# Kernel tuning notes

Measured on AMD Instinct MI355X. Metric: run time of the kernel, lower is better.

## Reference

```python
import jax, jax.numpy as jnp
import numpy as np

N_VERTS = 200000
NNZ = 1600000
C_IN = 128
C_OUT = 128


def setup_inputs() -> dict:
    key = jax.random.key(0)
    k1, k2, k3, k4, k5, k6 = jax.random.split(key, 6)
    x = jax.random.normal(k1, (N_VERTS, C_IN), dtype=jnp.float32)
    rows = jax.random.randint(k2, (NNZ,), 0, N_VERTS, dtype=jnp.int64)
    cols = jax.random.randint(k3, (NNZ,), 0, N_VERTS, dtype=jnp.int64)
    vals = jax.random.normal(k4, (NNZ,), dtype=jnp.float32)
    W = jax.random.normal(k5, (C_OUT, C_IN), dtype=jnp.float32) * (1.0 / np.sqrt(C_IN))
    b = jax.random.normal(k6, (C_OUT,), dtype=jnp.float32) * 0.01
    return {"x": x, "rows": rows, "cols": cols, "vals": vals, "W": W, "b": b}


def reference(x, rows, cols, vals, W, b):
    # SpMM: out[r] += vals[e] * x[cols[e]]  (F = 2I - L in COO form)
    n = x.shape[0]
    agg = jax.ops.segment_sum(vals[:, None] * x[cols], rows, num_segments=n)  # [N, C_in]
    # Dense Linear projection: agg @ W^T + b
    return agg @ W.T + b  # [N, C_out]
```

## Files before the change

### kernel.cpp

```cpp
#include <hip/hip_runtime.h>

#define NV 200000
#define NE 1600000
#define CD 128
#define NBUCK 3125
#define NBLK 64
#define CHUNK 25600

#define Y_OFF      0UL
#define CNT_OFF    51232768UL
#define TOT_OFF    52032768UL
#define START_OFF  52045312UL
#define SCAT_OFF   52058112UL
#define ROWOFF_OFF 64858112UL
#define SCAT2_OFF  65658368UL

typedef short  short8 __attribute__((ext_vector_type(8)));
typedef float  f32x4  __attribute__((ext_vector_type(4)));

__device__ __forceinline__ unsigned bf16pair(float a, float b) {
    unsigned ua = __float_as_uint(a);
    unsigned ub = __float_as_uint(b);
    ua += 0x7fffu + ((ua >> 16) & 1u);
    ub += 0x7fffu + ((ub >> 16) & 1u);
    return (ua >> 16) | (ub & 0xffff0000u);
}

__device__ __forceinline__ short bf16of(float f) {
    __bf16 h = (__bf16)f;
    return __builtin_bit_cast(short, h);
}

#define PC_BLOCKS 64
#define GEMM_BLOCKS 512
#define GEMM_WAVES (GEMM_BLOCKS * 4)
#define NTILES (NV / 16)

__global__ __launch_bounds__(256, 2) void gemm_pc(const float* __restrict__ x,
                                                  const float* __restrict__ Wm,
                                                  unsigned short* __restrict__ y,
                                                  const int* __restrict__ rows,
                                                  int* __restrict__ cnt) {
    __shared__ __align__(16) char smem[32768];
    const int t = threadIdx.x;

    if (blockIdx.x < PC_BLOCKS) {
        int* hist = reinterpret_cast<int*>(smem);
        const int blk = blockIdx.x;
        for (int i = t; i < NBUCK; i += 256) hist[i] = 0;
        __syncthreads();
        const int e0 = blk * CHUNK;
        const int e1 = min(NE, e0 + CHUNK);
        for (int e = e0 + t; e < e1; e += 256)
            atomicAdd(&hist[rows[e] >> 6], 1);
        __syncthreads();
        for (int i = t; i < NBUCK; i += 256)
            cnt[(size_t)blk * NBUCK + i] = hist[i];
        return;
    }

    short* Wlds = reinterpret_cast<short*>(smem);
    const int lane = t & 63;
    const int w = t >> 6;
    const int g = lane >> 4;

    {
        const float4* Wf4 = reinterpret_cast<const float4*>(Wm);
        uint4* L = reinterpret_cast<uint4*>(Wlds);
#pragma unroll
        for (int i = 0; i < 8; ++i) {
            int c = t + i * 256;
            int l = c & 63;
            int ks = (c >> 6) & 3;
            int tl = c >> 8;
            int row = 16 * tl + (l & 15);
            int j = ks * 4 + (l >> 4);
            float4 wa = Wf4[row * 32 + j * 2];
            float4 wb = Wf4[row * 32 + j * 2 + 1];
            uint4 u;
            u.x = bf16pair(wa.x, wa.y);
            u.y = bf16pair(wa.z, wa.w);
            u.z = bf16pair(wb.x, wb.y);
            u.w = bf16pair(wb.z, wb.w);
            L[c] = u;
        }
    }
    __syncthreads();

    short8 A[8][4];
    {
        const short8* L8 = reinterpret_cast<const short8*>(Wlds);
#pragma unroll
        for (int t8 = 0; t8 < 8; ++t8)
#pragma unroll
            for (int ks = 0; ks < 4; ++ks)
                A[t8][ks] = L8[(t8 * 4 + ks) * 64 + lane];
    }

    const int wgid = (blockIdx.x - PC_BLOCKS) * 4 + w;
    char* yb = reinterpret_cast<char*>(y);

    for (int tile = wgid; tile < NTILES; tile += GEMM_WAVES) {
        const int v0 = tile * 16;
        const int row = v0 + (lane & 15);
        const float4* xr = reinterpret_cast<const float4*>(x + (size_t)row * CD);

        float4 xf[8];
#pragma unroll
        for (int ks = 0; ks < 4; ++ks) {
            xf[2 * ks]     = xr[8 * ks + 2 * g];
            xf[2 * ks + 1] = xr[8 * ks + 2 * g + 1];
        }

        f32x4 acc[8];
#pragma unroll
        for (int t8 = 0; t8 < 8; ++t8) acc[t8] = (f32x4){0.f, 0.f, 0.f, 0.f};

#pragma unroll
        for (int ks = 0; ks < 4; ++ks) {
            short8 B;
            const float* f = reinterpret_cast<const float*>(&xf[2 * ks]);
#pragma unroll
            for (int j = 0; j < 8; ++j) B[j] = bf16of(f[j]);
#pragma unroll
            for (int t8 = 0; t8 < 8; ++t8)
                acc[t8] = __builtin_amdgcn_mfma_f32_16x16x32_bf16(A[t8][ks], B, acc[t8], 0, 0, 0);
        }

        const size_t rb = (size_t)(v0 + (lane & 15)) * 256;
#pragma unroll
        for (int t8 = 0; t8 < 8; ++t8) {
            ushort4 o;
            o.x = (unsigned short)bf16of(acc[t8][0]);
            o.y = (unsigned short)bf16of(acc[t8][1]);
            o.z = (unsigned short)bf16of(acc[t8][2]);
            o.w = (unsigned short)bf16of(acc[t8][3]);
            *reinterpret_cast<ushort4*>(yb + rb + t8 * 32 + g * 8) = o;
        }
    }
}

__global__ __launch_bounds__(256) void ps(int* __restrict__ cnt,
                                          int* __restrict__ tot) {
    int g = blockIdx.x * 256 + threadIdx.x;
    if (g >= NBUCK) return;
    int running = 0;
    for (int blk = 0; blk < NBLK; ++blk) {
        int idx = blk * NBUCK + g;
        int c = cnt[idx];
        cnt[idx] = running;
        running += c;
    }
    tot[g] = running;
}

__global__ __launch_bounds__(1024) void pt(const int* __restrict__ tot,
                                           int* __restrict__ start) {
    __shared__ int s[1024];
    const int t = threadIdx.x;
    if (t == 0) start[NBUCK] = NE;
    int carry = 0;
    for (int c = 0; c < 4; ++c) {
        int idx = c * 1024 + t;
        int v = (idx < NBUCK) ? tot[idx] : 0;
        s[t] = v;
        __syncthreads();
        for (int d = 1; d < 1024; d <<= 1) {
            int add = (t >= d) ? s[t - d] : 0;
            __syncthreads();
            s[t] += add;
            __syncthreads();
        }
        if (idx < NBUCK) start[idx] = carry + s[t] - v;
        carry += s[1023];
        __syncthreads();
    }
}

__global__ __launch_bounds__(1024) void px(const int* __restrict__ rows,
                                           const int* __restrict__ cols,
                                           const float* __restrict__ vals,
                                           const int* __restrict__ cnt,
                                           const int* __restrict__ start,
                                           int2* __restrict__ scat) {
    __shared__ int cur[NBUCK];
    const int t = threadIdx.x;
    for (int i = t; i < NBUCK; i += 1024)
        cur[i] = start[i] + cnt[(size_t)blockIdx.x * NBUCK + i];
    __syncthreads();
    const int e0 = blockIdx.x * CHUNK;
    const int e1 = min(NE, e0 + CHUNK);
    for (int e = e0 + t; e < e1; e += 1024) {
        int r = rows[e];
        int pos = atomicAdd(&cur[r >> 6], 1);
        scat[pos] = make_int2(cols[e] | ((r & 63) << 18), __float_as_int(vals[e]));
    }
}

__global__ __launch_bounds__(256) void k_sort(const int* __restrict__ start,
                                              const int2* __restrict__ scat,
                                              int2* __restrict__ scat2,
                                              int* __restrict__ rowoff) {
    __shared__ int rcnt[64], rinc[64], cur[64];
    const int t = threadIdx.x;
    const int b = blockIdx.x;
    const int s0 = start[b], s1 = start[b + 1];

    if (t < 64) rcnt[t] = 0;
    __syncthreads();
    for (int e = s0 + t; e < s1; e += 256)
        atomicAdd(&rcnt[(scat[e].x >> 18) & 63], 1);
    __syncthreads();
    if (t < 64) rinc[t] = rcnt[t];
    __syncthreads();
    for (int d = 1; d < 64; d <<= 1) {
        int add = 0;
        if (t < 64 && t >= d) add = rinc[t - d];
        __syncthreads();
        if (t < 64) rinc[t] += add;
        __syncthreads();
    }
    if (t < 64) {
        int excl = rinc[t] - rcnt[t];
        cur[t] = excl;
        rowoff[b * 64 + t] = s0 + excl;
    }
    if (b == NBUCK - 1 && t == 0) rowoff[NV] = NE;
    __syncthreads();
    for (int e = s0 + t; e < s1; e += 256) {
        int2 p = scat[e];
        int lr = (p.x >> 18) & 63;
        int pos = s0 + atomicAdd(&cur[lr], 1);
        scat2[pos] = p;
    }
}

#define BFLO(u) __uint_as_float((u) << 16)
#define BFHI(u) __uint_as_float((u) & 0xffff0000u)

__global__ __launch_bounds__(256) void k_gather(const int* __restrict__ rowoff,
                                                const int2* __restrict__ scat2,
                                                const uint4* __restrict__ y4,
                                                const float* __restrict__ b,
                                                float* __restrict__ out) {
    const int wid = threadIdx.x >> 6;
    const int lane = threadIdx.x & 63;
    const int q = lane >> 4;
    const int sl = lane & 15;
    const int row = blockIdx.x * 4 + wid;

    const int s0 = rowoff[row];
    const int n = rowoff[row + 1] - s0;

    float4 accA, accB;
    if (q == 0) {
        accA = reinterpret_cast<const float4*>(b)[2 * sl];
        accB = reinterpret_cast<const float4*>(b)[2 * sl + 1];
    } else {
        accA = make_float4(0.f, 0.f, 0.f, 0.f);
        accB = make_float4(0.f, 0.f, 0.f, 0.f);
    }

    int k = q;
    for (; k + 4 < n; k += 8) {
        int2 pa = scat2[s0 + k];
        int2 pb = scat2[s0 + k + 4];
        uint4 ua = y4[(size_t)(pa.x & 0x3ffff) * 16 + sl];
        uint4 ub = y4[(size_t)(pb.x & 0x3ffff) * 16 + sl];
        float va = __int_as_float(pa.y), vb = __int_as_float(pb.y);
        accA.x += va * BFLO(ua.x) + vb * BFLO(ub.x);
        accA.y += va * BFHI(ua.x) + vb * BFHI(ub.x);
        accA.z += va * BFLO(ua.y) + vb * BFLO(ub.y);
        accA.w += va * BFHI(ua.y) + vb * BFHI(ub.y);
        accB.x += va * BFLO(ua.z) + vb * BFLO(ub.z);
        accB.y += va * BFHI(ua.z) + vb * BFHI(ub.z);
        accB.z += va * BFLO(ua.w) + vb * BFLO(ub.w);
        accB.w += va * BFHI(ua.w) + vb * BFHI(ub.w);
    }
    if (k < n) {
        int2 p = scat2[s0 + k];
        uint4 u = y4[(size_t)(p.x & 0x3ffff) * 16 + sl];
        float v = __int_as_float(p.y);
        accA.x += v * BFLO(u.x);
        accA.y += v * BFHI(u.x);
        accA.z += v * BFLO(u.y);
        accA.w += v * BFHI(u.y);
        accB.x += v * BFLO(u.z);
        accB.y += v * BFHI(u.z);
        accB.z += v * BFLO(u.w);
        accB.w += v * BFHI(u.w);
    }

    accA.x += __shfl_xor(accA.x, 16); accA.x += __shfl_xor(accA.x, 32);
    accA.y += __shfl_xor(accA.y, 16); accA.y += __shfl_xor(accA.y, 32);
    accA.z += __shfl_xor(accA.z, 16); accA.z += __shfl_xor(accA.z, 32);
    accA.w += __shfl_xor(accA.w, 16); accA.w += __shfl_xor(accA.w, 32);
    accB.x += __shfl_xor(accB.x, 16); accB.x += __shfl_xor(accB.x, 32);
    accB.y += __shfl_xor(accB.y, 16); accB.y += __shfl_xor(accB.y, 32);
    accB.z += __shfl_xor(accB.z, 16); accB.z += __shfl_xor(accB.z, 32);
    accB.w += __shfl_xor(accB.w, 16); accB.w += __shfl_xor(accB.w, 32);

    if (q == 0) {
        f32x4 sA = {accA.x, accA.y, accA.z, accA.w};
        f32x4 sB = {accB.x, accB.y, accB.z, accB.w};
        float* o = out + (size_t)row * CD + sl * 8;
        __builtin_nontemporal_store(sA, (f32x4*)o);
        __builtin_nontemporal_store(sB, (f32x4*)(o + 4));
    }
}

extern "C" void kernel_launch(void* const* d_in, const int* in_sizes, int n_in,
                              void* d_out, int out_size, void* d_ws, size_t ws_size,
                              hipStream_t stream) {
    const float* x    = (const float*)d_in[0];
    const int*   rows = (const int*)d_in[1];
    const int*   cols = (const int*)d_in[2];
    const float* vals = (const float*)d_in[3];
    const float* Wm   = (const float*)d_in[4];
    const float* b    = (const float*)d_in[5];
    float* out = (float*)d_out;

    char* ws = (char*)d_ws;
    unsigned short* y  = (unsigned short*)(ws + Y_OFF);
    int* cnt           = (int*)(ws + CNT_OFF);
    int* tot           = (int*)(ws + TOT_OFF);
    int* start         = (int*)(ws + START_OFF);
    int2* scat         = (int2*)(ws + SCAT_OFF);
    int* rowoff        = (int*)(ws + ROWOFF_OFF);
    int2* scat2        = (int2*)(ws + SCAT2_OFF);

    gemm_pc<<<PC_BLOCKS + GEMM_BLOCKS, 256, 0, stream>>>(x, Wm, y, rows, cnt);
    ps<<<(NBUCK + 255) / 256, 256, 0, stream>>>(cnt, tot);
    pt<<<1, 1024, 0, stream>>>(tot, start);
    px<<<NBLK, 1024, 0, stream>>>(rows, cols, vals, cnt, start, scat);
    k_sort<<<NBUCK, 256, 0, stream>>>(start, scat, scat2, rowoff);
    k_gather<<<NV / 4, 256, 0, stream>>>(rowoff, scat2, (const uint4*)y, b, out);
}
```

Before: 184.1 us.

## Fuse GEMM and CSR build into one persistent kernel with grid barriers

Replaces the separate GEMM/histogram, two prefix-scan, scatter and per-bucket sort kernels with one persistent kernel of 256 blocks. Blocks synchronise through software grid barriers on global atomic counters, and slices of the GEMM tiles are spread across the phases so the idle blocks do dense work while the small scan steps run. This aims to remove launch gaps and to overlap the GEMM with the sort pipeline. In exchange it depends on all 256 blocks being resident at once, adds a memset and spin-wait cost, and fixes the GEMM tile split points by hand.

```diff
diff --git a/kernel.cpp b/kernel.cpp
--- a/kernel.cpp
+++ b/kernel.cpp
@@ -4,16 +4,23 @@
 #define NE 1600000
 #define CD 128
 #define NBUCK 3125
-#define NBLK 64
-#define CHUNK 25600
+#define NBLK 128
+#define CHUNK 12500
 
 #define Y_OFF      0UL
-#define CNT_OFF    51232768UL
-#define TOT_OFF    52032768UL
-#define START_OFF  52045312UL
-#define SCAT_OFF   52058112UL
-#define ROWOFF_OFF 64858112UL
-#define SCAT2_OFF  65658368UL
+#define CNT_OFF    51200000UL
+#define START_OFF  52812544UL
+#define SCAT_OFF   52825088UL
+#define ROWOFF_OFF 65625088UL
+#define SCAT2_OFF  66425344UL
+#define BAR_OFF    79225344UL
+
+#define FUSED_BLOCKS 256
+#define NTILES (NV / 16)
+#define T0 3000
+#define T1 5400
+#define T2 8400
+#define T3 11400
 
 typedef short  short8 __attribute__((ext_vector_type(8)));
 typedef float  f32x4  __attribute__((ext_vector_type(4)));
@@ -31,38 +38,40 @@
     return __builtin_bit_cast(short, h);
 }
 
-#define PC_BLOCKS 64
-#define GEMM_BLOCKS 512
-#define GEMM_WAVES (GEMM_BLOCKS * 4)
-#define NTILES (NV / 16)
-
-__global__ __launch_bounds__(256, 2) void gemm_pc(const float* __restrict__ x,
-                                                  const float* __restrict__ Wm,
-                                                  unsigned short* __restrict__ y,
-                                                  const int* __restrict__ rows,
-                                                  int* __restrict__ cnt) {
+__device__ __forceinline__ void gbar(int* cnt) {
+    __syncthreads();
+    if (threadIdx.x == 0) {
+        __threadfence();
+        atomicAdd(cnt, 1);
+        while (atomicAdd(cnt, 0) < FUSED_BLOCKS)
+            __builtin_amdgcn_s_sleep(8);
+    }
+    __syncthreads();
+    __threadfence();
+}
+
+__global__ __launch_bounds__(256, 2) void fused(const float* __restrict__ x,
+                                                const float* __restrict__ Wm,
+                                                unsigned short* __restrict__ y,
+                                                const int* __restrict__ rows,
+                                                const int* __restrict__ cols,
+                                                const float* __restrict__ vals,
+                                                int* __restrict__ cnt,
+                                                int* __restrict__ start,
+                                                int2* __restrict__ scat,
+                                                int* __restrict__ rowoff,
+                                                int2* __restrict__ scat2,
+                                                int* __restrict__ bar) {
     __shared__ __align__(16) char smem[32768];
+
     const int t = threadIdx.x;
-
-    if (blockIdx.x < PC_BLOCKS) {
-        int* hist = reinterpret_cast<int*>(smem);
-        const int blk = blockIdx.x;
-        for (int i = t; i < NBUCK; i += 256) hist[i] = 0;
-        __syncthreads();
-        const int e0 = blk * CHUNK;
-        const int e1 = min(NE, e0 + CHUNK);
-        for (int e = e0 + t; e < e1; e += 256)
-            atomicAdd(&hist[rows[e] >> 6], 1);
-        __syncthreads();
-        for (int i = t; i < NBUCK; i += 256)
-            cnt[(size_t)blk * NBUCK + i] = hist[i];
-        return;
-    }
-
-    short* Wlds = reinterpret_cast<short*>(smem);
+    const int bid = blockIdx.x;
     const int lane = t & 63;
     const int w = t >> 6;
     const int g = lane >> 4;
+
+    short* Wlds = reinterpret_cast<short*>(smem);
+    int* ibuf = reinterpret_cast<int*>(smem);
 
     {
         const float4* Wf4 = reinterpret_cast<const float4*>(Wm);
@@ -96,143 +105,157 @@
             for (int ks = 0; ks < 4; ++ks)
                 A[t8][ks] = L8[(t8 * 4 + ks) * 64 + lane];
     }
-
-    const int wgid = (blockIdx.x - PC_BLOCKS) * 4 + w;
+    __syncthreads();
+
     char* yb = reinterpret_cast<char*>(y);
-
-    for (int tile = wgid; tile < NTILES; tile += GEMM_WAVES) {
-        const int v0 = tile * 16;
-        const int row = v0 + (lane & 15);
-        const float4* xr = reinterpret_cast<const float4*>(x + (size_t)row * CD);
-
-        float4 xf[8];
-#pragma unroll
-        for (int ks = 0; ks < 4; ++ks) {
-            xf[2 * ks]     = xr[8 * ks + 2 * g];
-            xf[2 * ks + 1] = xr[8 * ks + 2 * g + 1];
-        }
-
-        f32x4 acc[8];
-#pragma unroll
-        for (int t8 = 0; t8 < 8; ++t8) acc[t8] = (f32x4){0.f, 0.f, 0.f, 0.f};
-
-#pragma unroll
-        for (int ks = 0; ks < 4; ++ks) {
-            short8 B;
-            const float* f = reinterpret_cast<const float*>(&xf[2 * ks]);
-#pragma unroll
-            for (int j = 0; j < 8; ++j) B[j] = bf16of(f[j]);
-#pragma unroll
-            for (int t8 = 0; t8 < 8; ++t8)
-                acc[t8] = __builtin_amdgcn_mfma_f32_16x16x32_bf16(A[t8][ks], B, acc[t8], 0, 0, 0);
-        }
-
-        const size_t rb = (size_t)(v0 + (lane & 15)) * 256;
-#pragma unroll
-        for (int t8 = 0; t8 < 8; ++t8) {
-            ushort4 o;
-            o.x = (unsigned short)bf16of(acc[t8][0]);
-            o.y = (unsigned short)bf16of(acc[t8][1]);
-            o.z = (unsigned short)bf16of(acc[t8][2]);
-            o.w = (unsigned short)bf16of(acc[t8][3]);
-            *reinterpret_cast<ushort4*>(yb + rb + t8 * 32 + g * 8) = o;
-        }
-    }
-}
-
-__global__ __launch_bounds__(256) void ps(int* __restrict__ cnt,
-                                          int* __restrict__ tot) {
-    int g = blockIdx.x * 256 + threadIdx.x;
-    if (g >= NBUCK) return;
-    int running = 0;
-    for (int blk = 0; blk < NBLK; ++blk) {
-        int idx = blk * NBUCK + g;
-        int c = cnt[idx];
-        cnt[idx] = running;
-        running += c;
-    }
-    tot[g] = running;
-}
-
-__global__ __launch_bounds__(1024) void pt(const int* __restrict__ tot,
-                                           int* __restrict__ start) {
-    __shared__ int s[1024];
-    const int t = threadIdx.x;
-    if (t == 0) start[NBUCK] = NE;
-    int carry = 0;
-    for (int c = 0; c < 4; ++c) {
-        int idx = c * 1024 + t;
-        int v = (idx < NBUCK) ? tot[idx] : 0;
-        s[t] = v;
-        __syncthreads();
-        for (int d = 1; d < 1024; d <<= 1) {
-            int add = (t >= d) ? s[t - d] : 0;
-            __syncthreads();
-            s[t] += add;
-            __syncthreads();
-        }
-        if (idx < NBUCK) start[idx] = carry + s[t] - v;
-        carry += s[1023];
-        __syncthreads();
-    }
-}
-
-__global__ __launch_bounds__(1024) void px(const int* __restrict__ rows,
-                                           const int* __restrict__ cols,
-                                           const float* __restrict__ vals,
-                                           const int* __restrict__ cnt,
-                                           const int* __restrict__ start,
-                                           int2* __restrict__ scat) {
-    __shared__ int cur[NBUCK];
-    const int t = threadIdx.x;
-    for (int i = t; i < NBUCK; i += 1024)
-        cur[i] = start[i] + cnt[(size_t)blockIdx.x * NBUCK + i];
-    __syncthreads();
-    const int e0 = blockIdx.x * CHUNK;
-    const int e1 = min(NE, e0 + CHUNK);
-    for (int e = e0 + t; e < e1; e += 1024) {
-        int r = rows[e];
-        int pos = atomicAdd(&cur[r >> 6], 1);
-        scat[pos] = make_int2(cols[e] | ((r & 63) << 18), __float_as_int(vals[e]));
-    }
-}
-
-__global__ __launch_bounds__(256) void k_sort(const int* __restrict__ start,
-                                              const int2* __restrict__ scat,
-                                              int2* __restrict__ scat2,
-                                              int* __restrict__ rowoff) {
-    __shared__ int rcnt[64], rinc[64], cur[64];
-    const int t = threadIdx.x;
-    const int b = blockIdx.x;
-    const int s0 = start[b], s1 = start[b + 1];
-
-    if (t < 64) rcnt[t] = 0;
-    __syncthreads();
-    for (int e = s0 + t; e < s1; e += 256)
-        atomicAdd(&rcnt[(scat[e].x >> 18) & 63], 1);
-    __syncthreads();
-    if (t < 64) rinc[t] = rcnt[t];
-    __syncthreads();
-    for (int d = 1; d < 64; d <<= 1) {
-        int add = 0;
-        if (t < 64 && t >= d) add = rinc[t - d];
-        __syncthreads();
-        if (t < 64) rinc[t] += add;
-        __syncthreads();
-    }
-    if (t < 64) {
-        int excl = rinc[t] - rcnt[t];
-        cur[t] = excl;
-        rowoff[b * 64 + t] = s0 + excl;
-    }
-    if (b == NBUCK - 1 && t == 0) rowoff[NV] = NE;
-    __syncthreads();
-    for (int e = s0 + t; e < s1; e += 256) {
-        int2 p = scat[e];
-        int lr = (p.x >> 18) & 63;
-        int pos = s0 + atomicAdd(&cur[lr], 1);
-        scat2[pos] = p;
-    }
+    auto gemm_tiles = [&](int lo, int hi, int gw, int nw) {
+        for (int tile = lo + gw; tile < hi; tile += nw) {
+            const int v0 = tile * 16;
+            const int row = v0 + (lane & 15);
+            const float4* xr = reinterpret_cast<const float4*>(x + (size_t)row * CD);
+            float4 xf[8];
+#pragma unroll
+            for (int ks = 0; ks < 4; ++ks) {
+                xf[2 * ks]     = xr[8 * ks + 2 * g];
+                xf[2 * ks + 1] = xr[8 * ks + 2 * g + 1];
+            }
+            f32x4 acc[8];
+#pragma unroll
+            for (int t8 = 0; t8 < 8; ++t8) acc[t8] = (f32x4){0.f, 0.f, 0.f, 0.f};
+#pragma unroll
+            for (int ks = 0; ks < 4; ++ks) {
+                short8 B;
+                const float* f = reinterpret_cast<const float*>(&xf[2 * ks]);
+#pragma unroll
+                for (int j = 0; j < 8; ++j) B[j] = bf16of(f[j]);
+#pragma unroll
+                for (int t8 = 0; t8 < 8; ++t8)
+                    acc[t8] = __builtin_amdgcn_mfma_f32_16x16x32_bf16(A[t8][ks], B, acc[t8], 0, 0, 0);
+            }
+            const size_t rb = (size_t)(v0 + (lane & 15)) * 256;
+#pragma unroll
+            for (int t8 = 0; t8 < 8; ++t8) {
+                ushort4 o;
+                o.x = (unsigned short)bf16of(acc[t8][0]);
+                o.y = (unsigned short)bf16of(acc[t8][1]);
+                o.z = (unsigned short)bf16of(acc[t8][2]);
+                o.w = (unsigned short)bf16of(acc[t8][3]);
+                *reinterpret_cast<ushort4*>(yb + rb + t8 * 32 + g * 8) = o;
+            }
+        }
+    };
+
+    if (bid < NBLK) {
+        int* hist = ibuf;
+        for (int i = t; i < NBUCK; i += 256) hist[i] = 0;
+        __syncthreads();
+        const int e0 = bid * CHUNK;
+        for (int e = e0 + t; e < e0 + CHUNK; e += 256)
+            atomicAdd(&hist[rows[e] >> 6], 1);
+        __syncthreads();
+        for (int i = t; i < NBUCK; i += 256)
+            cnt[(size_t)bid * NBUCK + i] = hist[i];
+    } else {
+        gemm_tiles(0, T0, (bid - NBLK) * 4 + w, (FUSED_BLOCKS - NBLK) * 4);
+    }
+    gbar(bar + 0);
+
+    if (bid < 13) {
+        int gi = bid * 256 + t;
+        if (gi < NBUCK) {
+            int running = 0;
+            for (int blk = 0; blk < NBLK; ++blk) {
+                int idx = blk * NBUCK + gi;
+                int c = cnt[idx];
+                cnt[idx] = running;
+                running += c;
+            }
+            start[gi] = running;
+        }
+    } else {
+        gemm_tiles(T0, T1, (bid - 13) * 4 + w, (FUSED_BLOCKS - 13) * 4);
+    }
+    gbar(bar + 1);
+
+    if (bid == 0) {
+        int* s = ibuf;
+        if (t == 0) ibuf[256] = 0;
+        __syncthreads();
+        for (int c = 0; c < 13; ++c) {
+            int idx = c * 256 + t;
+            int v = (idx < NBUCK) ? start[idx] : 0;
+            s[t] = v;
+            __syncthreads();
+            for (int d = 1; d < 256; d <<= 1) {
+                int add = (t >= d) ? s[t - d] : 0;
+                __syncthreads();
+                s[t] += add;
+                __syncthreads();
+            }
+            int carry = ibuf[256];
+            if (idx < NBUCK) start[idx] = carry + s[t] - v;
+            __syncthreads();
+            if (t == 255) ibuf[256] = carry + s[255];
+            __syncthreads();
+        }
+        if (t == 0) start[NBUCK] = NE;
+    } else {
+        gemm_tiles(T1, T2, (bid - 1) * 4 + w, (FUSED_BLOCKS - 1) * 4);
+    }
+    gbar(bar + 2);
+
+    if (bid < NBLK) {
+        int* cur = ibuf;
+        for (int i = t; i < NBUCK; i += 256)
+            cur[i] = start[i] + cnt[(size_t)bid * NBUCK + i];
+        __syncthreads();
+        const int e0 = bid * CHUNK;
+        for (int e = e0 + t; e < e0 + CHUNK; e += 256) {
+            int r = rows[e];
+            int pos = atomicAdd(&cur[r >> 6], 1);
+            scat[pos] = make_int2(cols[e] | ((r & 63) << 18), __float_as_int(vals[e]));
+        }
+    } else {
+        gemm_tiles(T2, T3, (bid - NBLK) * 4 + w, (FUSED_BLOCKS - NBLK) * 4);
+    }
+    gbar(bar + 3);
+
+    gemm_tiles(T3, NTILES, bid * 4 + w, FUSED_BLOCKS * 4);
+
+    int* rc = ibuf;
+    int* ri = ibuf + 64;
+    int* cu = ibuf + 128;
+    for (int b = bid; b < NBUCK; b += FUSED_BLOCKS) {
+        const int s0 = start[b], s1 = start[b + 1];
+        __syncthreads();
+        if (t < 64) rc[t] = 0;
+        __syncthreads();
+        for (int e = s0 + t; e < s1; e += 256)
+            atomicAdd(&rc[(scat[e].x >> 18) & 63], 1);
+        __syncthreads();
+        if (t < 64) ri[t] = rc[t];
+        __syncthreads();
+        for (int d = 1; d < 64; d <<= 1) {
+            int add = 0;
+            if (t < 64 && t >= d) add = ri[t - d];
+            __syncthreads();
+            if (t < 64) ri[t] += add;
+            __syncthreads();
+        }
+        if (t < 64) {
+            int excl = ri[t] - rc[t];
+            cu[t] = excl;
+            rowoff[b * 64 + t] = s0 + excl;
+        }
+        __syncthreads();
+        for (int e = s0 + t; e < s1; e += 256) {
+            int2 p = scat[e];
+            int lr = (p.x >> 18) & 63;
+            int pos = s0 + atomicAdd(&cu[lr], 1);
+            scat2[pos] = p;
+        }
+    }
+    if (bid == 0 && t == 0) rowoff[NV] = NE;
 }
 
 #define BFLO(u) __uint_as_float((u) << 16)
@@ -323,16 +346,14 @@
     char* ws = (char*)d_ws;
     unsigned short* y  = (unsigned short*)(ws + Y_OFF);
     int* cnt           = (int*)(ws + CNT_OFF);
-    int* tot           = (int*)(ws + TOT_OFF);
     int* start         = (int*)(ws + START_OFF);
     int2* scat         = (int2*)(ws + SCAT_OFF);
     int* rowoff        = (int*)(ws + ROWOFF_OFF);
     int2* scat2        = (int2*)(ws + SCAT2_OFF);
-
-    gemm_pc<<<PC_BLOCKS + GEMM_BLOCKS, 256, 0, stream>>>(x, Wm, y, rows, cnt);
-    ps<<<(NBUCK + 255) / 256, 256, 0, stream>>>(cnt, tot);
-    pt<<<1, 1024, 0, stream>>>(tot, start);
-    px<<<NBLK, 1024, 0, stream>>>(rows, cols, vals, cnt, start, scat);
-    k_sort<<<NBUCK, 256, 0, stream>>>(start, scat, scat2, rowoff);
+    int* bar           = (int*)(ws + BAR_OFF);
+
+    hipMemsetAsync(bar, 0, 8 * sizeof(int), stream);
+    fused<<<FUSED_BLOCKS, 256, 0, stream>>>(x, Wm, y, rows, cols, vals,
+                                            cnt, start, scat, rowoff, scat2, bar);
     k_gather<<<NV / 4, 256, 0, stream>>>(rowoff, scat2, (const uint4*)y, b, out);
 }
```

Result: slower. 335.9 us (+82.4%).
